# Kernel optimization log

Measured on AMD Instinct MI355X. Metric: run time of the kernel, lower is better.

## Reference

```python
import jax, jax.numpy as jnp
import numpy as np

B, N, D, E, H = 8, 256, 128, 32, 4
HD = D // H
EPS = 1e-5


def setup_inputs() -> dict:
    key = jax.random.key(0)
    ks = jax.random.split(key, 20)
    idx = jnp.arange(N)

    h = jax.random.normal(ks[0], (B, N, D), dtype=jnp.float32)
    adj = (jax.random.uniform(ks[1], (B, N, N)) < 0.5).astype(jnp.float32)
    adj = adj.at[:, idx, idx].set(1.0)
    edge_features = jax.random.normal(ks[2], (B, N, N, E), dtype=jnp.float32)
    src_mask = (jax.random.uniform(ks[3], (B, N, N)) < 0.7).astype(jnp.float32)
    src_mask = src_mask.at[:, idx, idx].set(1.0)

    s = 1.0 / np.sqrt(D)
    se = 1.0 / np.sqrt(E)
    p = {
        "gcn_w": jax.random.normal(ks[4], (D, D)) * s,
        "gcn_b": jnp.zeros((D,)),
        "edge_w": jax.random.normal(ks[5], (D, E)) * se,
        "edge_b": jnp.zeros((D,)),
        "wq": jax.random.normal(ks[6], (D, D)) * s,
        "wk": jax.random.normal(ks[7], (D, D)) * s,
        "wv": jax.random.normal(ks[8], (D, D)) * s,
        "bq": jnp.zeros((D,)),
        "bk": jnp.zeros((D,)),
        "bv": jnp.zeros((D,)),
        "out_w": jax.random.normal(ks[9], (D, D)) * s,
        "out_b": jnp.zeros((D,)),
        "ln_g": jnp.ones((D,)),
        "ln_b": jnp.zeros((D,)),
    }
    return {"h": h, "adj": adj, "edge_features": edge_features, "src_mask": src_mask, **p}


def reference(h, adj, edge_features, src_mask,
              gcn_w, gcn_b, edge_w, edge_b,
              wq, wk, wv, bq, bk, bv, out_w, out_b, ln_g, ln_b):
    b, n, d = h.shape

    # --- GCN branch: degree-normalized aggregation with self-loops ---
    adj_sl = adj + jnp.eye(n, dtype=h.dtype)[None]          # (B,N,N)
    deg = adj_sl.sum(-1, keepdims=True)                      # (B,N,1)
    h_agg = jnp.einsum('bnm,bmd->bnd', adj_sl, h) / deg
    h_gcn = h_agg @ gcn_w.T + gcn_b                          # (B,N,D)

    # --- edge-conditioned key/value: h_ij = h_j + edge_emb ---
    edge_emb = jnp.einsum('bnme,de->bnmd', edge_features, edge_w) + edge_b
    h_ij = h[:, None, :, :] + edge_emb                       # (B,N,N,D)

    # key padding mask: True where edge absent (masked)
    masked = (adj * src_mask) == 0                           # (B,N,N)

    # --- multi-head attention, one query per node ---
    q = (h @ wq.T + bq).reshape(b, n, H, HD)                 # (B,N,H,HD)
    k = (jnp.einsum('bnmd,ed->bnme', h_ij, wk) + bk).reshape(b, n, n, H, HD)
    v = (jnp.einsum('bnmd,ed->bnme', h_ij, wv) + bv).reshape(b, n, n, H, HD)

    scores = jnp.einsum('bnhd,bnmhd->bnhm', q, k) / np.sqrt(HD)  # (B,N,H,N)
    scores = jnp.where(masked[:, :, None, :], -jnp.inf, scores)
    attn = jax.nn.softmax(scores, axis=-1)
    o = jnp.einsum('bnhm,bnmhd->bnhd', attn, v).reshape(b, n, d)
    o = o @ out_w.T + out_b                                  # (B,N,D)

    # residual + layernorm (dropout is identity in eval)
    x = h + o
    mu = x.mean(-1, keepdims=True)
    var = ((x - mu) ** 2).mean(-1, keepdims=True)
    h_attn = ln_g * (x - mu) / jnp.sqrt(var + EPS) + ln_b

    return h_gcn + h_attn
```

## Files before the change

kernel.cpp:

```cpp
#include <hip/hip_runtime.h>
#include <hip/hip_bf16.h>

#define OFF_WQT 0
#define OFF_WKT 16384
#define OFF_WVT 32768
#define OFF_OWT 49152
#define OFF_GWT 65536
#define OFF_WKE 81920
#define OFF_WVET 86016
#define OFF_KB  90112
#define OFF_VB  90240
#define OFF_SC  90368
#define OFF_QSP 98560
#define OFF_QEP 229632
#define OFF_HG  360704
#define OFF_K0P 622848
#define OFF_V0P 753920

using half2_t = __attribute__((ext_vector_type(2))) __fp16;

static __device__ __forceinline__ half2_t u2h(unsigned int u){
  union { unsigned int u; half2_t h; } x; x.u = u; return x.h;
}
static __device__ __forceinline__ unsigned int pkf16(float a, float b){
  union { half2_t h; unsigned int u; } x;
  x.h = __builtin_amdgcn_cvt_pkrtz(a, b);
  return x.u;
}
static __device__ __forceinline__ float fdot2(unsigned int a, unsigned int b, float c){
  return __builtin_amdgcn_fdot2(u2h(a), u2h(b), c, false);
}

__global__ __launch_bounds__(256) void prep_kernel(
    const float* __restrict__ wq, const float* __restrict__ wk,
    const float* __restrict__ wv, const float* __restrict__ out_w,
    const float* __restrict__ gcn_w, const float* __restrict__ edge_w,
    const float* __restrict__ edge_b, const float* __restrict__ bk,
    const float* __restrict__ bv, float* __restrict__ ws)
{
  int blk = blockIdx.x, t = threadIdx.x;
  if (blk < 320) {
    int w = blk >> 6;
    int e0 = (blk & 63) * 256 + t;
    const float* src = (w==0) ? wq : (w==1) ? wk : (w==2) ? wv : (w==3) ? out_w : gcn_w;
    float* dst = ws + ((w==0) ? OFF_WQT : (w==1) ? OFF_WKT : (w==2) ? OFF_WVT
                      : (w==3) ? OFF_OWT : OFF_GWT);
    int k = e0 >> 7, d = e0 & 127;
    dst[e0] = src[d*128 + k];
  } else if (blk < 352) {
    int idx = blk - 320;
    int which = idx >> 4;
    int e0 = (idx & 15) * 256 + t;
    int dd = e0 >> 5, e = e0 & 31;
    const float* W = which ? wv : wk;
    float acc = 0.f;
    #pragma unroll 4
    for (int k2 = 0; k2 < 128; ++k2) acc += W[dd*128+k2] * edge_w[k2*32+e];
    if (which) ws[OFF_WVET + e*128 + dd] = acc;
    else       ws[OFF_WKE + e0] = acc;
  } else {
    int dd = t & 127;
    const float* W  = (t < 128) ? wk : wv;
    const float* bb = (t < 128) ? bk : bv;
    float acc = bb[dd];
    #pragma unroll 4
    for (int k2 = 0; k2 < 128; ++k2) acc += W[dd*128+k2] * edge_b[k2];
    ws[((t < 128) ? OFF_KB : OFF_VB) + dd] = acc;
  }
}

__global__ __launch_bounds__(256) void proj_kernel(
    const float* __restrict__ h, const float* __restrict__ adj,
    const float* __restrict__ bq, const float* __restrict__ gcn_b,
    float* __restrict__ ws)
{
  __shared__ float h_lds[256];
  __shared__ float adj_lds[512];
  __shared__ float p1[2][2][128];
  __shared__ float p2[2][2][128];
  __shared__ float p3[2][2][128];
  __shared__ float qrow[2*132];
  __shared__ float qe_l[2*132];
  __shared__ float dpart[2][2];
  __shared__ float ha_lds[2*132];

  int t = threadIdx.x;
  int d = t & 127, kh = t >> 7;
  int r0 = blockIdx.x * 2;
  int b  = r0 >> 8, n0 = r0 & 255;
  unsigned int* wsu = (unsigned int*)ws;

  if (t < 64)  ((float4*)h_lds)[t]   = ((const float4*)(h   + (size_t)r0*128))[t];
  if (t < 128) ((float4*)adj_lds)[t] = ((const float4*)(adj + (size_t)r0*256))[t];
  __syncthreads();

  {
    const float* wqT = ws + OFF_WQT;
    const float* wkT = ws + OFF_WKT;
    const float* wvT = ws + OFF_WVT;
    float aq0=0,aq1=0,ak0=0,ak1=0,av0=0,av1=0;
    #pragma unroll 4
    for (int kk = 0; kk < 64; ++kk) {
      int k = kh*64 + kk;
      float qw = wqT[k*128+d], kw = wkT[k*128+d], vw = wvT[k*128+d];
      float h0 = h_lds[k], h1 = h_lds[128+k];
      aq0 += qw*h0; aq1 += qw*h1;
      ak0 += kw*h0; ak1 += kw*h1;
      av0 += vw*h0; av1 += vw*h1;
    }
    p1[kh][0][d]=aq0; p1[kh][1][d]=aq1;
    p2[kh][0][d]=ak0; p2[kh][1][d]=ak1;
    p3[kh][0][d]=av0; p3[kh][1][d]=av1;
  }
  __syncthreads();

  {
    int i = t >> 7, dd = t & 127;
    const float inv = 0.17677669529663687f;
    qrow[i*132 + dd] = (p1[0][i][dd] + p1[1][i][dd] + bq[dd]) * inv;
  }
  {
    int i = (t >> 6) & 1, pr = t & 63;
    if (t < 128) {
      float k0 = p2[0][i][2*pr] + p2[1][i][2*pr];
      float k1 = p2[0][i][2*pr+1] + p2[1][i][2*pr+1];
      wsu[OFF_K0P + (size_t)(r0+i)*64 + pr] = pkf16(k0, k1);
    } else {
      float v0 = p3[0][i][2*pr] + p3[1][i][2*pr];
      float v1 = p3[0][i][2*pr+1] + p3[1][i][2*pr+1];
      wsu[OFF_V0P + (size_t)(r0+i)*64 + pr] = pkf16(v0, v1);
    }
  }
  __syncthreads();

  if (t < 128) {
    int i = t >> 6, pr = t & 63;
    wsu[OFF_QSP + (size_t)(r0+i)*64 + pr] = pkf16(qrow[i*132 + 2*pr], qrow[i*132 + 2*pr+1]);
  }
  {
    int i = t >> 7, he = t & 127, hh = he >> 5, e = he & 31;
    float acc = 0.f;
    #pragma unroll
    for (int j = 0; j < 32; ++j)
      acc += ws[OFF_WKE + (hh*32 + j)*32 + e] * qrow[i*132 + hh*32 + j];
    qe_l[i*132 + he] = acc;
  }
  if (t < 8) {
    int i = t >> 2, hh = t & 3;
    float acc = 0.f;
    #pragma unroll
    for (int j = 0; j < 32; ++j)
      acc += qrow[i*132 + hh*32 + j] * ws[OFF_KB + hh*32 + j];
    ws[OFF_SC + (size_t)(r0+i)*4 + hh] = acc;
  }
  {
    float ag0=0, ag1=0, dg0=0, dg1=0;
    #pragma unroll 4
    for (int mm = 0; mm < 128; ++mm) {
      int ml = kh*128 + mm;
      float hv = h[((size_t)b*256 + ml)*128 + d];
      float a0 = adj_lds[ml]       + ((ml == n0)     ? 1.0f : 0.0f);
      float a1 = adj_lds[256 + ml] + ((ml == n0 + 1) ? 1.0f : 0.0f);
      ag0 += a0*hv; ag1 += a1*hv; dg0 += a0; dg1 += a1;
    }
    p1[kh][0][d]=ag0; p1[kh][1][d]=ag1;
    if (d == 0) { dpart[kh][0]=dg0; dpart[kh][1]=dg1; }
  }
  __syncthreads();

  if (t < 128) {
    int i = t >> 6, pr = t & 63;
    wsu[OFF_QEP + (size_t)(r0+i)*64 + pr] = pkf16(qe_l[i*132 + 2*pr], qe_l[i*132 + 2*pr+1]);
  }
  {
    int i = t >> 7, dd = t & 127;
    ha_lds[i*132 + dd] = (p1[0][i][dd] + p1[1][i][dd]) / (dpart[0][i] + dpart[1][i]);
  }
  __syncthreads();

  {
    const float* gwT = ws + OFF_GWT;
    float g0=0, g1=0;
    #pragma unroll 4
    for (int kk = 0; kk < 64; ++kk) {
      int k = kh*64 + kk;
      float gw = gwT[k*128+d];
      g0 += gw * ha_lds[k];
      g1 += gw * ha_lds[132 + k];
    }
    p2[kh][0][d]=g0; p2[kh][1][d]=g1;
  }
  __syncthreads();
  {
    int i = t >> 7, dd = t & 127;
    ws[OFF_HG + (size_t)(r0+i)*128 + dd] = p2[0][i][dd] + p2[1][i][dd] + gcn_b[dd];
  }
}

__global__ __launch_bounds__(256) void attn_kernel(
    const float* __restrict__ edge, const float* __restrict__ adj,
    const float* __restrict__ srcm, const float* __restrict__ h,
    const float* __restrict__ out_b, const float* __restrict__ ln_g,
    const float* __restrict__ ln_b, const float* __restrict__ ws,
    float* __restrict__ out)
{
  __shared__ unsigned int e_buf[2*64*18];
  __shared__ unsigned int q_lds[128];
  __shared__ float s_chunk[4*66];
  __shared__ float wpart[16];
  __shared__ float ovh[128];
  __shared__ float eb_l[128];
  __shared__ float ov_l[128];
  __shared__ float o_l[128];
  __shared__ float px[256];
  __shared__ float stat[4];

  const int t  = threadIdx.x;
  const int bn = blockIdx.x;
  const int b  = bn >> 8;
  const int hh = t & 3;
  const int mq = t >> 2;
  const unsigned int* wsu = (const unsigned int*)ws;

  const float4* et = (const float4*)(edge + (size_t)bn*8192);

  float4 va = et[t];
  float4 vb = et[256 + t];
  float mp0 = adj[(size_t)bn*256 +       mq] * srcm[(size_t)bn*256 +       mq];
  float mp1 = adj[(size_t)bn*256 +  64 + mq] * srcm[(size_t)bn*256 +  64 + mq];
  float mp2 = adj[(size_t)bn*256 + 128 + mq] * srcm[(size_t)bn*256 + 128 + mq];
  float mp3 = adj[(size_t)bn*256 + 192 + mq] * srcm[(size_t)bn*256 + 192 + mq];

  if (t < 64)       q_lds[t]      = wsu[OFF_QSP + (size_t)bn*64 + t];
  else if (t < 128) q_lds[t]      = wsu[OFF_QEP + (size_t)bn*64 + (t - 64)];

  float sconst = ws[OFF_SC + (size_t)bn*4 + hh];
  const unsigned int* K0 = wsu + OFF_K0P + (size_t)b*256*64;

  float h_pre = 0.f, hg_pre = 0.f;
  if (t < 128) {
    h_pre  = h[(size_t)bn*128 + t];
    hg_pre = ws[OFF_HG + (size_t)bn*128 + t];
  }

  float exacc = 0.f;
  float acc4 = 0.f;
  float acc5x = 0.f, acc5y = 0.f;

  #pragma unroll
  for (int c = 0; c < 4; ++c) {
    unsigned int* eb = e_buf + (c & 1)*64*18;
    {
      int lr = t >> 3, c4 = t & 7;
      uint2 pk;
      pk.x = pkf16(va.x, va.y); pk.y = pkf16(va.z, va.w);
      *(uint2*)(eb + lr*18 + c4*2) = pk;
      uint2 pk2;
      pk2.x = pkf16(vb.x, vb.y); pk2.y = pkf16(vb.z, vb.w);
      *(uint2*)(eb + (32 + lr)*18 + c4*2) = pk2;
    }
    if (c < 3) {
      va = et[(c+1)*512 + t];
      vb = et[(c+1)*512 + 256 + t];
    }
    __syncthreads();

    {
      int gm = c*64 + mq;
      float acc = sconst;
      const uint4* kr4 = (const uint4*)(K0 + (size_t)gm*64 + hh*16);
      const uint4* qs4 = (const uint4*)(q_lds + hh*16);
      const uint4* qe4 = (const uint4*)(q_lds + 64 + hh*16);
      #pragma unroll
      for (int j4 = 0; j4 < 4; ++j4) {
        uint4 kw = kr4[j4];
        uint4 qw = qs4[j4];
        acc = fdot2(qw.x, kw.x, acc);
        acc = fdot2(qw.y, kw.y, acc);
        acc = fdot2(qw.z, kw.z, acc);
        acc = fdot2(qw.w, kw.w, acc);
      }
      const uint2* er = (const uint2*)(eb + mq*18);
      #pragma unroll
      for (int j4 = 0; j4 < 4; ++j4) {
        uint4 qw = qe4[j4];
        uint2 w0 = er[2*j4], w1 = er[2*j4+1];
        acc = fdot2(qw.x, w0.x, acc);
        acc = fdot2(qw.y, w0.y, acc);
        acc = fdot2(qw.z, w1.x, acc);
        acc = fdot2(qw.w, w1.y, acc);
      }
      float mp = (c==0) ? mp0 : (c==1) ? mp1 : (c==2) ? mp2 : mp3;
      float ex = (mp == 0.0f) ? 0.0f : __expf(acc);
      s_chunk[hh*66 + mq] = ex;
      exacc += ex;
    }
    __syncthreads();

    if (t < 128) {
      int e = t & 31, ht = t >> 5;
      const float* sc_ = s_chunk + ht*66;
      const unsigned int* ebr = eb + (e >> 1);
      bool hi = (e & 1);
      float a0 = 0.f, a1 = 0.f;
      #pragma unroll 8
      for (int m = 0; m < 64; m += 2) {
        float s0 = sc_[m], s1 = sc_[m+1];
        half2_t w0 = u2h(ebr[m*18]);
        half2_t w1 = u2h(ebr[(m+1)*18]);
        float e0 = hi ? (float)w0.y : (float)w0.x;
        float e1 = hi ? (float)w1.y : (float)w1.x;
        a0 += s0*e0; a1 += s1*e1;
      }
      acc4 += a0 + a1;
    } else {
      int idx = t - 128;
      int j = idx & 63, mh = idx >> 6;
      int head = j >> 4;
      const float* sc_ = s_chunk + head*66 + mh*32;
      const unsigned int* vp = wsu + OFF_V0P + ((size_t)b*256 + c*64 + mh*32)*64 + j;
      float a0 = 0.f, a1 = 0.f;
      #pragma unroll 8
      for (int m = 0; m < 32; ++m) {
        float s = sc_[m];
        half2_t v = u2h(vp[(size_t)m*64]);
        a0 += s*(float)v.x; a1 += s*(float)v.y;
      }
      acc5x += a0; acc5y += a1;
    }
  }

  exacc += __shfl_down(exacc, 4);
  exacc += __shfl_down(exacc, 8);
  exacc += __shfl_down(exacc, 16);
  exacc += __shfl_down(exacc, 32);
  if ((t & 63) < 4) wpart[(t >> 6)*4 + hh] = exacc;
  if (t >= 192) {
    int j = (t - 128) & 63;
    float2 p; p.x = acc5x; p.y = acc5y;
    *(float2*)(ovh + j*2) = p;
  }
  __syncthreads();

  if (t < 128) {
    int ht = t >> 5;
    float inv = 1.0f / (wpart[ht] + wpart[4+ht] + wpart[8+ht] + wpart[12+ht]);
    eb_l[t] = acc4 * inv;
  } else if (t < 192) {
    int j = t - 128, head = j >> 4;
    float inv = 1.0f / (wpart[head] + wpart[4+head] + wpart[8+head] + wpart[12+head]);
    float2 oh = *(const float2*)(ovh + j*2);
    float2 res;
    res.x = (acc5x + oh.x)*inv + ws[OFF_VB + 2*j];
    res.y = (acc5y + oh.y)*inv + ws[OFF_VB + 2*j + 1];
    *(float2*)(ov_l + 2*j) = res;
  }
  __syncthreads();

  if (t < 128) {
    int hd = t >> 5;
    float acc = ov_l[t];
    const float* wveT = ws + OFF_WVET;
    #pragma unroll 8
    for (int e = 0; e < 32; ++e) acc += wveT[e*128 + t] * eb_l[hd*32 + e];
    o_l[t] = acc;
  }
  __syncthreads();

  {
    int d = t & 127, kh = t >> 7;
    const float* owT = ws + OFF_OWT;
    float xa = 0.f;
    #pragma unroll 8
    for (int kk = 0; kk < 64; ++kk) {
      int k = kh*64 + kk;
      xa += owT[k*128 + d] * o_l[k];
    }
    px[kh*128 + d] = xa;
  }
  __syncthreads();

  float x = 0.f;
  if (t < 128) {
    x = px[t] + px[128 + t] + out_b[t] + h_pre;
    float s = x, ss = x*x;
    #pragma unroll
    for (int off = 32; off > 0; off >>= 1) {
      s  += __shfl_down(s,  off);
      ss += __shfl_down(ss, off);
    }
    if ((t & 63) == 0) { stat[t >> 6] = s; stat[2 + (t >> 6)] = ss; }
  }
  __syncthreads();

  if (t < 128) {
    float mu   = (stat[0] + stat[1]) * (1.0f/128.0f);
    float var  = (stat[2] + stat[3]) * (1.0f/128.0f) - mu*mu;
    float rstd = rsqrtf(var + 1e-5f);
    out[(size_t)bn*128 + t] =
        ln_g[t]*(x - mu)*rstd + ln_b[t] + hg_pre;
  }
}

extern "C" void kernel_launch(void* const* d_in, const int* in_sizes, int n_in,
                              void* d_out, int out_size, void* d_ws, size_t ws_size,
                              hipStream_t stream) {
  (void)in_sizes; (void)n_in; (void)out_size; (void)ws_size;
  const float* h     = (const float*)d_in[0];
  const float* adj   = (const float*)d_in[1];
  const float* edge  = (const float*)d_in[2];
  const float* srcm  = (const float*)d_in[3];
  const float* gcn_w = (const float*)d_in[4];
  const float* gcn_b = (const float*)d_in[5];
  const float* edge_w= (const float*)d_in[6];
  const float* edge_b= (const float*)d_in[7];
  const float* wq    = (const float*)d_in[8];
  const float* wk    = (const float*)d_in[9];
  const float* wv    = (const float*)d_in[10];
  const float* bq    = (const float*)d_in[11];
  const float* bk    = (const float*)d_in[12];
  const float* bv    = (const float*)d_in[13];
  const float* out_w = (const float*)d_in[14];
  const float* out_b = (const float*)d_in[15];
  const float* ln_g  = (const float*)d_in[16];
  const float* ln_b  = (const float*)d_in[17];

  float* ws  = (float*)d_ws;
  float* out = (float*)d_out;

  prep_kernel<<<353, 256, 0, stream>>>(wq, wk, wv, out_w, gcn_w, edge_w, edge_b, bk, bv, ws);
  proj_kernel<<<1024, 256, 0, stream>>>(h, adj, bq, gcn_b, ws);
  attn_kernel<<<2048, 256, 0, stream>>>(edge, adj, srcm, h, out_b, ln_g, ln_b, ws, out);
}
```

Before: 184.7 us.

## Software-pipeline attention chunks so scoring overlaps the previous chunk's aggregation

Restructures the chunk loop of the attention kernel into a software pipeline. The score computation for chunk c now runs in the same barrier phase as the edge and V aggregation for chunk c-1 and the fp16 packing of chunk c+1. A triple-buffered edge LDS and double-buffered score array allow this, which cuts the barriers from two per chunk to one. The cost is more shared memory per block and a prologue and epilogue, which could lower occupancy.

```diff
diff --git a/kernel.cpp b/kernel.cpp
--- a/kernel.cpp
+++ b/kernel.cpp
@@ -204,9 +204,9 @@
     const float* __restrict__ ln_b, const float* __restrict__ ws,
     float* __restrict__ out)
 {
-  __shared__ unsigned int e_buf[2*64*18];
+  __shared__ unsigned int e_buf[3*64*18];
   __shared__ unsigned int q_lds[128];
-  __shared__ float s_chunk[4*66];
+  __shared__ float s_chunk[2][4*66];
   __shared__ float wpart[16];
   __shared__ float ovh[128];
   __shared__ float eb_l[128];
@@ -231,8 +231,8 @@
   float mp2 = adj[(size_t)bn*256 + 128 + mq] * srcm[(size_t)bn*256 + 128 + mq];
   float mp3 = adj[(size_t)bn*256 + 192 + mq] * srcm[(size_t)bn*256 + 192 + mq];
 
-  if (t < 64)       q_lds[t]      = wsu[OFF_QSP + (size_t)bn*64 + t];
-  else if (t < 128) q_lds[t]      = wsu[OFF_QEP + (size_t)bn*64 + (t - 64)];
+  if (t < 64)       q_lds[t] = wsu[OFF_QSP + (size_t)bn*64 + t];
+  else if (t < 128) q_lds[t] = wsu[OFF_QEP + (size_t)bn*64 + (t - 64)];
 
   float sconst = ws[OFF_SC + (size_t)bn*4 + hh];
   const unsigned int* K0 = wsu + OFF_K0P + (size_t)b*256*64;
@@ -242,6 +242,19 @@
     h_pre  = h[(size_t)bn*128 + t];
     hg_pre = ws[OFF_HG + (size_t)bn*128 + t];
   }
+
+  {
+    int lr = t >> 3, c4 = t & 7;
+    uint2 pk;
+    pk.x = pkf16(va.x, va.y); pk.y = pkf16(va.z, va.w);
+    *(uint2*)(e_buf + lr*18 + c4*2) = pk;
+    uint2 pk2;
+    pk2.x = pkf16(vb.x, vb.y); pk2.y = pkf16(vb.z, vb.w);
+    *(uint2*)(e_buf + (32 + lr)*18 + c4*2) = pk2;
+  }
+  va = et[512 + t];
+  vb = et[768 + t];
+  __syncthreads();
 
   float exacc = 0.f;
   float acc4 = 0.f;
@@ -249,21 +262,7 @@
 
   #pragma unroll
   for (int c = 0; c < 4; ++c) {
-    unsigned int* eb = e_buf + (c & 1)*64*18;
-    {
-      int lr = t >> 3, c4 = t & 7;
-      uint2 pk;
-      pk.x = pkf16(va.x, va.y); pk.y = pkf16(va.z, va.w);
-      *(uint2*)(eb + lr*18 + c4*2) = pk;
-      uint2 pk2;
-      pk2.x = pkf16(vb.x, vb.y); pk2.y = pkf16(vb.z, vb.w);
-      *(uint2*)(eb + (32 + lr)*18 + c4*2) = pk2;
-    }
-    if (c < 3) {
-      va = et[(c+1)*512 + t];
-      vb = et[(c+1)*512 + 256 + t];
-    }
-    __syncthreads();
+    const unsigned int* ebc = e_buf + (c % 3)*64*18;
 
     {
       int gm = c*64 + mq;
@@ -280,7 +279,7 @@
         acc = fdot2(qw.z, kw.z, acc);
         acc = fdot2(qw.w, kw.w, acc);
       }
-      const uint2* er = (const uint2*)(eb + mq*18);
+      const uint2* er = (const uint2*)(ebc + mq*18);
       #pragma unroll
       for (int j4 = 0; j4 < 4; ++j4) {
         uint4 qw = qe4[j4];
@@ -292,15 +291,76 @@
       }
       float mp = (c==0) ? mp0 : (c==1) ? mp1 : (c==2) ? mp2 : mp3;
       float ex = (mp == 0.0f) ? 0.0f : __expf(acc);
-      s_chunk[hh*66 + mq] = ex;
+      s_chunk[c & 1][hh*66 + mq] = ex;
       exacc += ex;
     }
+
+    if (c > 0) {
+      const unsigned int* ebp = e_buf + ((c-1) % 3)*64*18;
+      const float* scp = s_chunk[(c-1) & 1];
+      if (t < 128) {
+        int e = t & 31, ht = t >> 5;
+        const float* sc_ = scp + ht*66;
+        const unsigned int* ebr = ebp + (e >> 1);
+        bool hi = (e & 1);
+        float a0 = 0.f, a1 = 0.f;
+        #pragma unroll 8
+        for (int m = 0; m < 64; m += 2) {
+          float s0 = sc_[m], s1 = sc_[m+1];
+          half2_t w0 = u2h(ebr[m*18]);
+          half2_t w1 = u2h(ebr[(m+1)*18]);
+          float e0 = hi ? (float)w0.y : (float)w0.x;
+          float e1 = hi ? (float)w1.y : (float)w1.x;
+          a0 += s0*e0; a1 += s1*e1;
+        }
+        acc4 += a0 + a1;
+      } else {
+        int idx = t - 128;
+        int j = idx & 63, mh = idx >> 6;
+        int head = j >> 4;
+        const float* sc_ = scp + head*66 + mh*32;
+        const unsigned int* vp = wsu + OFF_V0P + ((size_t)b*256 + (c-1)*64 + mh*32)*64 + j;
+        float a0 = 0.f, a1 = 0.f;
+        #pragma unroll 8
+        for (int m = 0; m < 32; ++m) {
+          float s = sc_[m];
+          half2_t v = u2h(vp[(size_t)m*64]);
+          a0 += s*(float)v.x; a1 += s*(float)v.y;
+        }
+        acc5x += a0; acc5y += a1;
+      }
+    }
+
+    if (c < 3) {
+      unsigned int* ebn = e_buf + ((c+1) % 3)*64*18;
+      int lr = t >> 3, c4 = t & 7;
+      uint2 pk;
+      pk.x = pkf16(va.x, va.y); pk.y = pkf16(va.z, va.w);
+      *(uint2*)(ebn + lr*18 + c4*2) = pk;
+      uint2 pk2;
+      pk2.x = pkf16(vb.x, vb.y); pk2.y = pkf16(vb.z, vb.w);
+      *(uint2*)(ebn + (32 + lr)*18 + c4*2) = pk2;
+      if (c < 2) {
+        va = et[(c+2)*512 + t];
+        vb = et[(c+2)*512 + 256 + t];
+      }
+    }
     __syncthreads();
-
+  }
+
+  exacc += __shfl_down(exacc, 4);
+  exacc += __shfl_down(exacc, 8);
+  exacc += __shfl_down(exacc, 16);
+  exacc += __shfl_down(exacc, 32);
+  if ((t & 63) < 4) wpart[(t >> 6)*4 + hh] = exacc;
+
+  {
+    const unsigned int* ebp = e_buf + (3 % 3)*64*18;
+    const float* scp = s_chunk[1];
     if (t < 128) {
       int e = t & 31, ht = t >> 5;
-      const float* sc_ = s_chunk + ht*66;
-      const unsigned int* ebr = eb + (e >> 1);
+      const float* sc_ = scp + ht*66;
+      const unsigned int* ebr = ebp + (e >> 1);
       bool hi = (e & 1);
       float a0 = 0.f, a1 = 0.f;
       #pragma unroll 8
@@ -317,8 +377,8 @@
       int idx = t - 128;
       int j = idx & 63, mh = idx >> 6;
       int head = j >> 4;
-      const float* sc_ = s_chunk + head*66 + mh*32;
-      const unsigned int* vp = wsu + OFF_V0P + ((size_t)b*256 + c*64 + mh*32)*64 + j;
+      const float* sc_ = scp + head*66 + mh*32;
+      const unsigned int* vp = wsu + OFF_V0P + ((size_t)b*256 + 192 + mh*32)*64 + j;
       float a0 = 0.f, a1 = 0.f;
       #pragma unroll 8
       for (int m = 0; m < 32; ++m) {
@@ -329,12 +389,6 @@
       acc5x += a0; acc5y += a1;
     }
   }
-
-  exacc += __shfl_down(exacc, 4);
-  exacc += __shfl_down(exacc, 8);
-  exacc += __shfl_down(exacc, 16);
-  exacc += __shfl_down(exacc, 32);
-  if ((t & 63) < 4) wpart[(t >> 6)*4 + hh] = exacc;
   if (t >= 192) {
     int j = (t - 128) & 63;
     float2 p; p.x = acc5x; p.y = acc5y;
```

After: 184.0 us. About the same (-0.4%).
